# Kernel optimization log

Measured on AMD Instinct MI355X. Metric: run time of the kernel, lower is better.

The kernel has to match this reference:

```python
import jax, jax.numpy as jnp
import numpy as np

CH, K, RR = 12, 7, 4  # pooled temporal size / involution kernel / reduction ratio

def conv3d(x, w, pad):
    return jax.lax.conv_general_dilated(x, w, (1, 1, 1), [(pad, pad)] * 3,
                                        dimension_numbers=('NCDHW', 'OIDHW', 'NCDHW'))

def conv1x1(x, w, b=None):
    out = jnp.einsum('oi,bidhw->bodhw', w, x)
    return out if b is None else out + b[None, :, None, None, None]

def adaptive_pool(x, outs):
    b, c, D, H, W = x.shape
    fd, fh, fw = D // outs[0], H // outs[1], W // outs[2]
    return x.reshape(b, c, outs[0], fd, outs[1], fh, outs[2], fw).mean(axis=(3, 5, 7))

def bnorm(x, g, b):
    m = x.mean(axis=(0, 2, 3, 4), keepdims=True)
    v = x.var(axis=(0, 2, 3, 4), keepdims=True)
    return (x - m) * jax.lax.rsqrt(v + 1e-5) * g[None, :, None, None, None] + b[None, :, None, None, None]

def setup_inputs():
    key = jax.random.key(0)
    ks = jax.random.split(key, 12)
    c = 64; cr = c // RR; Cf = c + CH * cr; M = CH * K * K
    def nrm(k_, shape, fan_in):
        return jax.random.normal(k_, shape, jnp.float32) / np.sqrt(fan_in)
    return {
        'x_CT': jax.random.normal(ks[0], (2, c, 8, 56, 56), jnp.float32),
        'x_WSI': jax.random.normal(ks[1], (2, c, 12, 56, 56), jnp.float32),
        'W_ct': nrm(ks[2], (c, c), c), 'b_ct': jnp.zeros((c,), jnp.float32),
        'W_wsi': nrm(ks[3], (c, c), c), 'b_wsi': jnp.zeros((c,), jnp.float32),
        'W_att': nrm(ks[4], (1 + CH, M, 5, 5, 5), M * 125),
        'W_inv': nrm(ks[5], (K * K, M), M), 'b_inv': jnp.zeros((K * K,), jnp.float32),
        'W_rr': nrm(ks[6], (cr, c, 3, 3, 3), c * 27),
        'g1': jnp.ones((Cf,), jnp.float32), 'be1': jnp.zeros((Cf,), jnp.float32),
        'g2': jnp.ones((Cf,), jnp.float32), 'be2': jnp.zeros((Cf,), jnp.float32),
        'W_p1': nrm(ks[7], (Cf, Cf), Cf), 'b_p1': jnp.zeros((Cf,), jnp.float32),
        'W_p2': nrm(ks[8], (c, Cf), Cf), 'b_p2': jnp.zeros((c,), jnp.float32),
    }

def reference(x_CT, x_WSI, W_ct, b_ct, W_wsi, b_wsi, W_att, W_inv, b_inv, W_rr,
              g1, be1, g2, be2, W_p1, b_p1, W_p2, b_p2):
    b, c, t, h, w = x_CT.shape
    cr = c // RR
    M = CH * K * K
    x1 = conv1x1(x_CT, W_ct, b_ct)
    xw1 = adaptive_pool(conv1x1(x_WSI, W_wsi, b_wsi), (CH, K, K))       # (b,c,CH,K,K)
    # cross-modal bmm: (b, thw, c) x (b, c, M) -> (b, thw, M)
    multi = jnp.einsum('bnc,bcm->bnm', x1.reshape(b, c, t * h * w).transpose(0, 2, 1),
                       xw1.reshape(b, c, M))
    feature = multi.reshape(b, t, h, w, M).transpose(0, 4, 1, 2, 3)     # (b,M,t,h,w)
    Att = jax.nn.sigmoid(conv3d(feature, W_att, 2))                      # (b,1+CH,t,h,w)
    xw3 = conv3d(x_WSI, W_rr, 1)                                         # (b,cr,CH,h,w)
    xw5 = jnp.broadcast_to(xw3.reshape(b, cr * CH, 1, h, w), (b, cr * CH, t, h, w))
    x_FS = jnp.concatenate([x_CT, xw5], axis=1)                          # (b,Cf,t,h,w)
    Att_CT = jnp.broadcast_to(Att[:, :1], (b, c, t, h, w))
    Att_WSI = jnp.tile(Att[:, 1:].reshape(b, CH, t, h * w), (1, 1, cr, 1)).reshape(b, CH * cr, t, h, w)
    Att_FS = jnp.concatenate([Att_CT, Att_WSI], axis=1)
    x_Att = x_FS * Att_FS + x_FS
    # per-pixel dynamic kernel: (b,t,K,K,h,w)
    kern = conv1x1(feature, W_inv, b_inv).transpose(0, 2, 1, 3, 4).reshape(b, t, K, K, h, w)
    x_Att1 = jax.nn.relu(bnorm(conv1x1(x_Att, W_p1, b_p1), g1, be1))
    pad = K // 2
    xp = jnp.pad(x_Att1, ((0, 0), (0, 0), (0, 0), (pad, pad), (pad, pad)))
    out = jnp.zeros_like(x_Att1)
    for i in range(K):                                                   # fixed 7x7 involution taps
        for j in range(K):
            out = out + kern[:, None, :, i, j] * xp[:, :, :, i:i + h, j:j + w]
    return conv1x1(bnorm(out, g2, be2) + x_Att, W_p2, b_p2)
```

## Files before the change

### kernel.cpp

```cpp
#include <hip/hip_runtime.h>
#include <hip/hip_bf16.h>
#include <hip/hip_fp16.h>
#include <math.h>

typedef __hip_bfloat16 bf16;
typedef unsigned short us;
typedef __attribute__((ext_vector_type(8))) short short8v;
typedef __attribute__((ext_vector_type(4))) float f32x4;
#define DEV static __device__ __forceinline__
DEV float b2f(bf16 x){ return __bfloat162float(x); }
DEV bf16  f2b(float x){ return __float2bfloat16(x); }
DEV us    f2u(float x){ bf16 h=f2b(x); return *(us*)&h; }
DEV float u2f(us u){ return __uint_as_float(((unsigned)u)<<16); }
DEV us    f2h(float x){ __half h=__float2half(x); return *(us*)&h; }
DEV float hlo(unsigned int w){ return __half2float(__ushort_as_half((us)(w&0xffff))); }
DEV float hhi(unsigned int w){ return __half2float(__ushort_as_half((us)(w>>16))); }
DEV float ldin(const void* p, long i, int f){
  return f ? ((const float*)p)[i] : b2f(((const bf16*)p)[i]);
}

#define PP 25088

#define POOLo  3211264L
#define XW1o   3286528L
#define WXo    3361792L
#define WXTo   3569792L
#define WIXo   3825792L
#define ATTo   3832064L
#define KERNo  4484352L
#define XW3o   6942976L
#define STATo  8147200L
#define FLAGo  8149248L
#define WFo    8149264L
#define WATTFo 8267280L
#define WINVFo 9222784L
#define BF16o  9251600L
#define WRR2o  WXo
#define bX1T   3211264L
#define bXATT  8028160L
#define bY1    20873216L
#define bINV   33718272L
#define bWP1B  46563328L
#define bWP2B  46628864L
#define bW2S   46645248L
#define bXWT   bY1
#define oWCT   0
#define oBCT   4096
#define oWWSI  4160
#define oBWSI  8256
#define oWRR   8320
#define oBINV  35968
#define oWP1   36032
#define oWP2   101568
#define oBP2   117952

__global__ void k_detect(const us* raw, int* flag){
  int t = threadIdx.x;
  us u = raw[2*t];
  int e = (u>>7)&0xFF;
  int hit = (e >= 137);
  unsigned long long m = __ballot(hit);
  if(t==0) flag[0] = (__popcll(m) >= 8) ? 1 : 0;
}

__global__ void k_c2f(const void* src, float* dst, int n, const int* flag){
  int i = blockIdx.x*256+threadIdx.x; if(i>=n) return;
  dst[i] = ldin(src, i, flag[0]);
}

__global__ void k_cvt(const void* Wct,const void* bct,const void* Wwsi,const void* bwsi,
                      const void* Wrr,const void* binv,const void* Wp1,const void* Wp2,
                      const void* bp2,float* wf,const int* flag){
  int i = blockIdx.x*256 + threadIdx.x;
  int f = flag[0];
  if (i < 4096){ int co=i>>6, ci=i&63; wf[oWCT + ci*64+co] = ldin(Wct,i,f); }
  else if (i < 4160){ wf[i] = ldin(bct,i-4096,f); }
  else if (i < 8256){ wf[i] = ldin(Wwsi,i-4160,f); }
  else if (i < 8320){ wf[i] = ldin(bwsi,i-8256,f); }
  else if (i < 35968){ int l=i-8320; int co=l/1728, r=l%1728, ci=r/27, tp=r%27;
                       wf[oWRR + (ci*27+tp)*16+co] = ldin(Wrr,l,f); }
  else if (i < 36017){ wf[oBINV + (i-35968)] = ldin(binv,i-35968,f); }
  else if (i < 36032){ }
  else if (i < 101568){ int l=i-36032; int co=l>>8, ci=l&255; wf[oWP1 + ci*256+co] = ldin(Wp1,l,f); }
  else if (i < 117952){ int l=i-101568; int o=l>>8, ci=l&255; wf[oWP2 + ci*64+o] = ldin(Wp2,l,f); }
  else if (i < 118016){ int l=i-117952; if(l<64) wf[oBP2 + l] = ldin(bp2,l,f); }
}

__global__ void k_wb(const void* Wp1, const void* Wp2, us* Wp1b, us* Wp2b, const int* flag){
  int i = blockIdx.x*256+threadIdx.x;
  int f = flag[0];
  if(i<65536) Wp1b[i]=f2u(ldin(Wp1,i,f));
  else if(i<81920) Wp2b[i-65536]=f2u(ldin(Wp2,i-65536,f));
}

__global__ void k_wsit(const void* xwsi_r, const int* flag, us* xwt){
  __shared__ us tl[64*68];
  int tid=threadIdx.x; int p0=blockIdx.x*64; int d=blockIdx.y; int b=blockIdx.z;
  int f=flag[0];
  #pragma unroll
  for(int k=0;k<16;k++){
    int idx=k*256+tid; int px=idx&63, c=idx>>6;
    float v = ldin(xwsi_r, ((long)(b*64+c)*12+d)*3136 + p0+px, f);
    tl[px*68+c] = f2u(v);
  }
  __syncthreads();
  #pragma unroll
  for(int k=0;k<16;k++){
    int idx=k*256+tid; int px=idx>>6, ch=idx&63;
    xwt[((size_t)(b*12+d)*3136 + p0+px)*64 + ch] = tl[px*68+ch];
  }
}

__global__ void k_pool(const us* xwt, float* pool){
  int i = blockIdx.x*256+threadIdx.x;
  int c = i&63; int m=(i>>6)%588; int b=i/37632;
  int d=m/49, r=m%49, ii=r/7, jj=r%7;
  const us* src = xwt + ((size_t)(b*12+d)*3136 + (ii*8)*56 + jj*8)*64 + c;
  float s=0;
  for(int u=0;u<8;u++)
    for(int v=0;v<8;v++) s += u2f(src[(size_t)(u*56+v)*64]);
  pool[i] = s*(1.f/64.f);
}

__global__ void k_xw1(const float* pool, const float* wf, float* xw1){
  int i = blockIdx.x*256+threadIdx.x;
  int c = i&63; int m=(i>>6)%588; int b=i/37632;
  const float* p = pool + (b*588+m)*64;
  const float* w = wf + oWWSI + c*64;
  float s = wf[oBWSI + c];
  for(int ci=0;ci<64;ci++) s += w[ci]*p[ci];
  xw1[i]=s;
}

__global__ void k_Wx(const float* Wattf, const float* xw1, float* Wx){
  int i = blockIdx.x*256+threadIdx.x; if(i>=208000) return;
  int c=i&63; int r=i>>6; int tap=r%125; int o=(r/125)%13; int b=r/1625;
  const float* wa = Wattf + (size_t)o*588*125 + tap;
  const float* xp = xw1 + b*588*64 + c;
  float s=0;
  for(int m=0;m<588;m++) s += wa[(size_t)m*125] * xp[m*64];
  Wx[i]=s;
}

__global__ void k_Wfrag(const float* Wx, us* Wf){
  int i = blockIdx.x*256+threadIdx.x; if(i>=256000) return;
  int j=i&7; int m=(i>>3)&15; int kg=(i>>7)&3; int ch=(i>>9)&1;
  int r=i>>10; int tap=r%125; int b=r/125;
  int c = ch*32 + kg*8 + j;
  float v = (m<13) ? Wx[((size_t)(b*13+m)*125+tap)*64 + c] : 0.f;
  Wf[i] = f2u(v);
}

__global__ void k_rrfrag(const float* wf, us* Wrr2){
  int i = blockIdx.x*256+threadIdx.x; if(i>=27648) return;
  int j=i&7; int l=(i>>3)&63; int kg=(i>>9)&1; int td=i>>10;
  int m=l&15, g=l>>4;
  int c = kg*32 + g*8 + j;
  Wrr2[i] = f2u(wf[oWRR + (c*27+td)*16 + m]);
}

__global__ void k_Winvx(const float* Winvf, const float* xw1, float* Wix){
  int i = blockIdx.x*256+threadIdx.x; if(i>=6272) return;
  int kk=i%49; int c=(i/49)&63; int b=i/3136;
  const float* xp = xw1 + b*588*64 + c;
  float s=0;
  for(int m=0;m<588;m++) s += Winvf[kk*588+m] * xp[m*64];
  Wix[i]=s;
}

__global__ void k_x1(const void* xct_r, const int* flag, const float* wf, us* x1t){
  int p = blockIdx.x*256+threadIdx.x;
  int co0 = blockIdx.y*16; int b = blockIdx.z;
  float acc[16];
  #pragma unroll
  for(int o=0;o<16;o++) acc[o]=wf[oBCT+co0+o];
  int f=flag[0];
  if(f){
    const float* xp = (const float*)xct_r + (size_t)b*64*PP + p;
    for(int ci=0;ci<64;ci++){
      float xv = xp[(size_t)ci*PP];
      const float* w = wf + oWCT + ci*64 + co0;
      #pragma unroll
      for(int o=0;o<16;o++) acc[o] += w[o]*xv;
    }
  } else {
    const bf16* xp = (const bf16*)xct_r + (size_t)b*64*PP + p;
    for(int ci=0;ci<64;ci++){
      float xv = b2f(xp[(size_t)ci*PP]);
      const float* w = wf + oWCT + ci*64 + co0;
      #pragma unroll
      for(int o=0;o<16;o++) acc[o] += w[o]*xv;
    }
  }
  unsigned int pk[8];
  #pragma unroll
  for(int o2=0;o2<8;o2++)
    pk[o2] = (unsigned)f2u(acc[2*o2]) | ((unsigned)f2u(acc[2*o2+1])<<16);
  us* xo = x1t + ((size_t)(b*PP)+p)*64 + co0;
  *(uint4*)xo     = make_uint4(pk[0],pk[1],pk[2],pk[3]);
  *(uint4*)(xo+8) = make_uint4(pk[4],pk[5],pk[6],pk[7]);
}

__global__ __launch_bounds__(256) void k_att(const us* x1t, const us* Wf, float* att){
  __shared__ short xt[10368];
  int tid=threadIdx.x;
  int tile=blockIdx.x, t=blockIdx.y, b=blockIdx.z;
  int y0=(tile/7)*8, x0=(tile%7)*8;
  int w=tid>>6, l=tid&63;
  int pc=l&7, pr=(l>>3)&1, g=l>>4;
  f32x4 acc0={0,0,0,0}, acc1={0,0,0,0};
  int bbase = ((2*w+pr)*12 + pc)*72 + g*8;
  const us* Wb = Wf + (size_t)b*128000 + l*8;
  for(int dt=0;dt<5;dt++){
    int ti=t+dt-2;
    if(ti<0||ti>=8) continue;
    __syncthreads();
    for(int e=tid;e<1152;e+=256){
      int px=e>>3, q=e&7;
      int row=px/12, col=px-row*12;
      int gy=y0+row-2, gx=x0+col-2;
      uint4 v={0,0,0,0};
      if((unsigned)gy<56u && (unsigned)gx<56u)
        v = *(const uint4*)(x1t + ((size_t)(b*PP) + ti*3136 + gy*56 + gx)*64 + q*8);
      *(uint4*)&xt[px*72 + q*8] = v;
    }
    __syncthreads();
    const us* Wd = Wb + dt*25600;
    #pragma unroll
    for(int dy=0;dy<5;dy++){
      #pragma unroll
      for(int dx=0;dx<5;dx++){
        int off = bbase + dy*864 + dx*72;
        short8v a0 = *(const short8v*)(Wd + (dy*5+dx)*1024);
        short8v b0 = *(const short8v*)&xt[off];
        acc0 = __builtin_amdgcn_mfma_f32_16x16x32_bf16(a0,b0,acc0,0,0,0);
        short8v a1 = *(const short8v*)(Wd + (dy*5+dx)*1024 + 512);
        short8v b1 = *(const short8v*)&xt[off+32];
        acc1 = __builtin_amdgcn_mfma_f32_16x16x32_bf16(a1,b1,acc1,0,0,0);
      }
    }
  }
  int px=l&15; int epc=px&7, epr=px>>3;
  size_t pbase=(size_t)t*3136+(size_t)(y0+2*w+epr)*56+x0+epc;
  #pragma unroll
  for(int r=0;r<4;r++){
    int o=g*4+r;
    if(o<13){
      float s=acc0[r]+acc1[r];
      att[((size_t)b*13+o)*PP+pbase]=1.f/(1.f+__expf(-s));
    }
  }
}

__global__ void k_kern(const us* x1t, const float* Wix, const float* wf, float* kern){
  int p = blockIdx.x*256+threadIdx.x; int b=blockIdx.y;
  float acc[49];
  #pragma unroll
  for(int kk=0;kk<49;kk++) acc[kk]=wf[oBINV+kk];
  const us* xp = x1t + ((size_t)b*PP + p)*64;
  #pragma unroll
  for(int c8=0;c8<8;c8++){
    uint4 v = *(const uint4*)(xp + c8*8);
    const us* vp=(const us*)&v;
    #pragma unroll
    for(int j=0;j<8;j++){
      float xv = u2f(vp[j]);
      const float* w = Wix + (b*64+c8*8+j)*49;
      #pragma unroll
      for(int kk=0;kk<49;kk++) acc[kk]+=w[kk]*xv;
    }
  }
  float* out = kern + (size_t)b*49*PP + p;
  #pragma unroll
  for(int kk=0;kk<49;kk++) out[(size_t)kk*PP]=acc[kk];
}

__global__ __launch_bounds__(256) void k_rr(const us* xwt, const us* Wrr2, bf16* xw3){
  __shared__ short xt[7200];
  int tid=threadIdx.x;
  int tile=blockIdx.x, d=blockIdx.y, b=blockIdx.z;
  int y0=(tile/7)*8, x0=(tile%7)*8;
  int w=tid>>6, l=tid&63;
  int pc=l&7, pr=(l>>3)&1, g=l>>4;
  f32x4 acc0={0,0,0,0}, acc1={0,0,0,0};
  int bbase = ((2*w+pr)*10 + pc)*72 + g*8;
  const us* Wl = Wrr2 + l*8;
  for(int dz=0;dz<3;dz++){
    int di=d+dz-1;
    if(di<0||di>=12) continue;
    __syncthreads();
    for(int e=tid;e<800;e+=256){
      int px=e>>3, q=e&7;
      int row=px/10, col=px-row*10;
      int gy=y0+row-1, gx=x0+col-1;
      uint4 v={0,0,0,0};
      if((unsigned)gy<56u && (unsigned)gx<56u)
        v = *(const uint4*)(xwt + ((size_t)(b*12+di)*3136 + gy*56 + gx)*64 + q*8);
      *(uint4*)&xt[px*72 + q*8] = v;
    }
    __syncthreads();
    const us* Wd = Wl + dz*9216;
    #pragma unroll
    for(int tap=0;tap<9;tap++){
      int dy=tap/3, dx=tap-dy*3;
      int off = bbase + (dy*10+dx)*72;
      short8v a0 = *(const short8v*)(Wd + tap*1024);
      short8v b0 = *(const short8v*)&xt[off];
      acc0 = __builtin_amdgcn_mfma_f32_16x16x32_bf16(a0,b0,acc0,0,0,0);
      short8v a1 = *(const short8v*)(Wd + tap*1024 + 512);
      short8v b1 = *(const short8v*)&xt[off+32];
      acc1 = __builtin_amdgcn_mfma_f32_16x16x32_bf16(a1,b1,acc1,0,0,0);
    }
  }
  int px=l&15; int epc=px&7, epr=px>>3;
  size_t pp=(size_t)(y0+2*w+epr)*56 + x0+epc;
  #pragma unroll
  for(int r=0;r<4;r++){
    int o=g*4+r;
    xw3[((size_t)(b*16+o)*12+d)*3136 + pp] = f2b(acc0[r]+acc1[r]);
  }
}

__global__ void k_xatt(const void* xct_r, const int* flag, const bf16* xw3,
                       const float* att, us* xattT){
  __shared__ us tl[64*258];
  int tid=threadIdx.x; int p0=blockIdx.x*64; int b=blockIdx.y;
  int f=flag[0];
  for(int k=0;k<64;k++){
    int idx=k*256+tid; int ch=idx>>6, pp=idx&63;
    int p=p0+pp;
    float v;
    if(ch<64){
      long ix = (long)(b*64+ch)*PP+p;
      float xv;
      if(f) xv = ((const float*)xct_r)[ix]; else xv = b2f(((const bf16*)xct_r)[ix]);
      v = xv * (1.f+att[(size_t)b*13*PP+p]);
    } else {
      int q=ch-64; int co=q/12, dd=q-co*12;
      int s=p%3136;
      v = b2f(xw3[((size_t)(b*16+co)*12+dd)*3136+s]) * (1.f+att[((size_t)b*13+1+q/16)*PP+p]);
    }
    tl[pp*258+ch]=f2u(v);
  }
  __syncthreads();
  for(int k=0;k<64;k++)
    xattT[((size_t)b*PP + p0+k)*256 + tid] = tl[k*258+tid];
}

__global__ __launch_bounds__(256) void k_p1(const us* xattT, const us* Wp1b, us* y1T){
  __shared__ us wt[16384];
  int tid=threadIdx.x; int w=tid>>6, l=tid&63;
  int pt=blockIdx.x, qtr=blockIdx.y, b=blockIdx.z;
  int co0 = qtr*64;
  #pragma unroll
  for(int it=0;it<8;it++){
    int f = it*256+tid;
    int n=f>>9, kc=(f>>6)&7, lane=f&63;
    int co = co0 + n*16 + (lane&15);
    int ci = (lane>>4)*8 + kc*32;
    uint4 v = *(const uint4*)(Wp1b + (size_t)co*256 + ci);
    *(uint4*)(wt + f*8) = v;
  }
  __syncthreads();
  int p0 = pt*64 + w*16;
  const us* xa = xattT + ((size_t)b*PP + p0 + (l&15))*256 + ((l>>4)*8);
  f32x4 acc[4];
  #pragma unroll
  for(int n=0;n<4;n++) acc[n]=(f32x4){0,0,0,0};
  for(int kc=0;kc<8;kc++){
    short8v a = *(const short8v*)(xa + kc*32);
    #pragma unroll
    for(int n=0;n<4;n++){
      short8v bf = *(const short8v*)(wt + ((n*8+kc)*64 + l)*8);
      acc[n] = __builtin_amdgcn_mfma_f32_16x16x32_bf16(a,bf,acc[n],0,0,0);
    }
  }
  int col=l&15, rowb=(l>>4)*4;
  us* yo = y1T + ((size_t)b*PP + p0)*256 + co0;
  #pragma unroll
  for(int n=0;n<4;n++)
    #pragma unroll
    for(int r=0;r<4;r++)
      yo[(size_t)(rowb+r)*256 + n*16 + col] = f2u(acc[n][r]);
}

__global__ void k_stats(const us* src, float* sum, float* sq){
  int tid=threadIdx.x; int pt=blockIdx.x, b=blockIdx.y;
  const us* p = src + ((size_t)b*PP + pt*64)*256 + tid;
  float s=0,q=0;
  #pragma unroll 8
  for(int i=0;i<64;i++){ float v=u2f(p[(size_t)i*256]); s+=v; q+=v*v; }
  atomicAdd(&sum[tid],s); atomicAdd(&sq[tid],q);
}
__global__ void k_finstat(const float* sum, const float* sq, const void* g, const void* be,
                          const int* flag, float* sc, float* sh){
  int ch=threadIdx.x;
  int f=flag[0];
  float m = sum[ch]*(1.f/50176.f);
  float v = sq[ch]*(1.f/50176.f) - m*m;
  float s = ldin(g,ch,f) * rsqrtf(v+1e-5f);
  sc[ch]=s; sh[ch]=ldin(be,ch,f) - m*s;
}

__global__ __launch_bounds__(256) void k_inv(const us* y1T, const float* sc1, const float* sh1,
                                             const float* kern, us* invT){
  __shared__ __align__(16) us xt[196*72];
  int tid=threadIdx.x;
  int bx=blockIdx.x, by=blockIdx.y, bz=blockIdx.z;
  int t=bz&7, b=bz>>3;
  int y0=(bx/7)*8, x0=(bx%7)*8, c0=by*64;
  int w=tid>>6, l=tid&63;
  int ty=l>>3, tx=l&7;
  int segb = c0 + (tid&7)*8;
  float scr[8], shr[8];
  #pragma unroll
  for(int j=0;j<8;j++){ scr[j]=sc1[segb+j]; shr[j]=sh1[segb+j]; }
  for(int e=tid;e<1568;e+=256){
    int row=e>>3, seg=e&7;
    int yy=row/14, xx=row%14;
    int gy=y0+yy-3, gx=x0+xx-3;
    uint4 o4={0,0,0,0};
    if(gy>=0&&gy<56&&gx>=0&&gx<56){
      uint4 v = *(const uint4*)&y1T[((size_t)b*PP + t*3136 + gy*56+gx)*256 + c0 + seg*8];
      const us* vp=(const us*)&v;
      us r[8];
      #pragma unroll
      for(int j=0;j<8;j++){
        float x = u2f(vp[j]);
        x = x*scr[j]+shr[j]; x = x>0.f?x:0.f;
        r[j]=f2h(x);
      }
      o4 = *(const uint4*)r;
    }
    *(uint4*)&xt[row*72+seg*8]=o4;
  }
  float kr[49];
  size_t pxs=(size_t)t*3136 + (y0+ty)*56 + x0+tx;
  #pragma unroll
  for(int kk=0;kk<49;kk++) kr[kk]=kern[((size_t)b*49+kk)*PP+pxs];
  __syncthreads();
  #pragma unroll
  for(int s=0;s<2;s++){
    int sub=2*w+s;
    float acc[8];
    #pragma unroll
    for(int e=0;e<8;e++) acc[e]=0;
    for(int i=0;i<7;i++){
      #pragma unroll
      for(int j=0;j<7;j++){
        uint4 u = *(const uint4*)&xt[((ty+i)*14+tx+j)*72 + sub*8];
        float kv = kr[i*7+j];
        acc[0]+=hlo(u.x)*kv; acc[1]+=hhi(u.x)*kv;
        acc[2]+=hlo(u.y)*kv; acc[3]+=hhi(u.y)*kv;
        acc[4]+=hlo(u.z)*kv; acc[5]+=hhi(u.z)*kv;
        acc[6]+=hlo(u.w)*kv; acc[7]+=hhi(u.w)*kv;
      }
    }
    unsigned pk[4];
    #pragma unroll
    for(int e=0;e<4;e++)
      pk[e] = (unsigned)f2u(acc[2*e]) | ((unsigned)f2u(acc[2*e+1])<<16);
    *(uint4*)&invT[((size_t)b*PP+pxs)*256 + c0 + sub*8] = make_uint4(pk[0],pk[1],pk[2],pk[3]);
  }
}

__global__ void k_w2s(const float* wf, const float* sc2, const float* sh2,
                      us* W2sb, float* bias2){
  __shared__ float red[256];
  int o=blockIdx.x, ci=threadIdx.x;
  float wv = wf[oWP2 + ci*64 + o];
  W2sb[o*256+ci] = f2u(wv * sc2[ci]);
  red[ci] = wv * sh2[ci];
  __syncthreads();
  for(int st=128;st>0;st>>=1){ if(ci<st) red[ci]+=red[ci+st]; __syncthreads(); }
  if(ci==0) bias2[o] = wf[oBP2+o] + red[0];
}

__global__ __launch_bounds__(256) void k_final(const us* invT, const us* xattT,
                                               const us* W2sb, const us* Wp2b,
                                               const float* bias2, float* out){
  __shared__ us wt[32768];
  int tid=threadIdx.x; int w=tid>>6, l=tid&63;
  int pt=blockIdx.x, b=blockIdx.y;
  #pragma unroll
  for(int it=0;it<16;it++){
    int f = it*256+tid;
    int which = f>>11;
    int g = f&2047;
    int n=g>>9, kc=(g>>6)&7, lane=g&63;
    int co = n*16 + (lane&15);
    int ci = (lane>>4)*8 + kc*32;
    const us* src = which ? Wp2b : W2sb;
    uint4 v = *(const uint4*)(src + (size_t)co*256 + ci);
    *(uint4*)(wt + f*8) = v;
  }
  __syncthreads();
  int p0 = pt*64 + w*16;
  size_t abase = ((size_t)b*PP + p0 + (l&15))*256 + ((l>>4)*8);
  f32x4 acc[4];
  #pragma unroll
  for(int n=0;n<4;n++) acc[n]=(f32x4){0,0,0,0};
  for(int kc=0;kc<8;kc++){
    short8v ai = *(const short8v*)(invT + abase + kc*32);
    short8v ax = *(const short8v*)(xattT + abase + kc*32);
    #pragma unroll
    for(int n=0;n<4;n++){
      short8v b1 = *(const short8v*)(wt + ((n*8+kc)*64 + l)*8);
      acc[n] = __builtin_amdgcn_mfma_f32_16x16x32_bf16(ai,b1,acc[n],0,0,0);
      short8v b2 = *(const short8v*)(wt + 16384 + ((n*8+kc)*64 + l)*8);
      acc[n] = __builtin_amdgcn_mfma_f32_16x16x32_bf16(ax,b2,acc[n],0,0,0);
    }
  }
  int col=l&15, rowb=(l>>4)*4;
  #pragma unroll
  for(int n=0;n<4;n++){
    float bb = bias2[n*16+col];
    #pragma unroll
    for(int r=0;r<4;r++)
      out[((size_t)b*64 + n*16+col)*PP + p0 + rowb + r] = acc[n][r] + bb;
  }
}

extern "C" void kernel_launch(void* const* d_in, const int* in_sizes, int n_in,
                              void* d_out, int out_size, void* d_ws, size_t ws_size,
                              hipStream_t stream){
  const void* xct_r =d_in[0];
  const void* xwsi_r=d_in[1];
  const void* Wct =d_in[2];
  const void* bct =d_in[3];
  const void* Wwsi=d_in[4];
  const void* bwsi=d_in[5];
  const void* Watt=d_in[6];
  const void* Winv=d_in[7];
  const void* binv=d_in[8];
  const void* Wrr =d_in[9];
  const void* g1  =d_in[10];
  const void* be1 =d_in[11];
  const void* g2  =d_in[12];
  const void* be2 =d_in[13];
  const void* Wp1 =d_in[14];
  const void* Wp2 =d_in[16];
  const void* bp2 =d_in[17];
  float* ws=(float*)d_ws;
  float* pool=ws+POOLo; float* xw1=ws+XW1o;
  float* Wx=ws+WXo; float* Wix=ws+WIXo;
  float* att=ws+ATTo; float* kern=ws+KERNo;
  us* Wf=(us*)(ws+WXTo);
  us* Wrr2=(us*)(ws+WRR2o);
  bf16* xw3=(bf16*)(ws+XW3o);
  float* stat=ws+STATo; float* wf=ws+WFo;
  float* Wattf=ws+WATTFo; float* Winvf=ws+WINVFo;
  float* bias2=ws+WATTFo;
  int* flag=(int*)(ws+FLAGo);
  bf16* bfb=(bf16*)(ws+BF16o);
  us* x1t=(us*)(bfb+bX1T);
  us* xattT=(us*)(bfb+bXATT); us* y1T=(us*)(bfb+bY1); us* invT=(us*)(bfb+bINV);
  us* Wp1b=(us*)(bfb+bWP1B); us* Wp2b=(us*)(bfb+bWP2B); us* W2sb=(us*)(bfb+bW2S);
  us* xwt=(us*)(bfb+bXWT);
  float* sum1=stat; float* sq1=stat+256; float* sum2=stat+512; float* sq2=stat+768;
  float* sc1=stat+1024; float* sh1=stat+1280; float* sc2=stat+1536; float* sh2=stat+1792;

  hipMemsetAsync(stat,0,4096,stream);
  k_detect<<<1,64,0,stream>>>((const us*)xct_r,flag);
  k_c2f   <<<3733,256,0,stream>>>(Watt,Wattf,955500,flag);
  k_c2f   <<<113,256,0,stream>>>(Winv,Winvf,28812,flag);
  k_cvt   <<<461,256,0,stream>>>(Wct,bct,Wwsi,bwsi,Wrr,binv,Wp1,Wp2,bp2,wf,flag);
  k_wb    <<<320,256,0,stream>>>(Wp1,Wp2,Wp1b,Wp2b,flag);
  k_wsit  <<<dim3(49,12,2),256,0,stream>>>(xwsi_r,flag,xwt);
  k_pool  <<<294,256,0,stream>>>(xwt,pool);
  k_xw1   <<<294,256,0,stream>>>(pool,wf,xw1);
  k_Wx    <<<813,256,0,stream>>>(Wattf,xw1,Wx);
  k_Wfrag <<<1000,256,0,stream>>>(Wx,Wf);
  k_rrfrag<<<108,256,0,stream>>>(wf,Wrr2);
  k_Winvx <<<25,256,0,stream>>>(Winvf,xw1,Wix);
  k_x1    <<<dim3(98,4,2),256,0,stream>>>(xct_r,flag,wf,x1t);
  k_att   <<<dim3(49,8,2),256,0,stream>>>(x1t,Wf,att);
  k_kern  <<<dim3(98,2),256,0,stream>>>(x1t,Wix,wf,kern);
  k_rr    <<<dim3(49,12,2),256,0,stream>>>(xwt,Wrr2,xw3);
  k_xatt  <<<dim3(392,2),256,0,stream>>>(xct_r,flag,xw3,att,xattT);
  k_p1    <<<dim3(392,4,2),256,0,stream>>>(xattT,Wp1b,y1T);
  k_stats <<<dim3(392,2),256,0,stream>>>(y1T,sum1,sq1);
  k_finstat<<<1,256,0,stream>>>(sum1,sq1,g1,be1,flag,sc1,sh1);
  k_inv   <<<dim3(49,4,16),256,0,stream>>>(y1T,sc1,sh1,kern,invT);
  k_stats <<<dim3(392,2),256,0,stream>>>(invT,sum2,sq2);
  k_finstat<<<1,256,0,stream>>>(sum2,sq2,g2,be2,flag,sc2,sh2);
  k_w2s   <<<64,256,0,stream>>>(wf,sc2,sh2,W2sb,bias2);
  k_final <<<dim3(392,2),256,0,stream>>>(invT,xattT,W2sb,Wp2b,bias2,(float*)d_out);
}
```

Before: 386.2 us.

## Merge weight-prep kernels, fuse pool with xw1, split Winvx and kern for parallelism

```diff
diff --git a/kernel.cpp b/kernel.cpp
--- a/kernel.cpp
+++ b/kernel.cpp
@@ -1,6 +1,5 @@
 #include <hip/hip_runtime.h>
 #include <hip/hip_bf16.h>
-#include <hip/hip_fp16.h>
 #include <math.h>
 
 typedef __hip_bfloat16 bf16;
@@ -12,9 +11,8 @@
 DEV bf16  f2b(float x){ return __float2bfloat16(x); }
 DEV us    f2u(float x){ bf16 h=f2b(x); return *(us*)&h; }
 DEV float u2f(us u){ return __uint_as_float(((unsigned)u)<<16); }
-DEV us    f2h(float x){ __half h=__float2half(x); return *(us*)&h; }
-DEV float hlo(unsigned int w){ return __half2float(__ushort_as_half((us)(w&0xffff))); }
-DEV float hhi(unsigned int w){ return __half2float(__ushort_as_half((us)(w>>16))); }
+DEV float blo(unsigned int w){ return __uint_as_float(w<<16); }
+DEV float bhi(unsigned int w){ return __uint_as_float(w&0xffff0000u); }
 DEV float ldin(const void* p, long i, int f){
   return f ? ((const float*)p)[i] : b2f(((const bf16*)p)[i]);
 }
@@ -63,16 +61,16 @@
   if(t==0) flag[0] = (__popcll(m) >= 8) ? 1 : 0;
 }
 
-__global__ void k_c2f(const void* src, float* dst, int n, const int* flag){
-  int i = blockIdx.x*256+threadIdx.x; if(i>=n) return;
-  dst[i] = ldin(src, i, flag[0]);
-}
-
-__global__ void k_cvt(const void* Wct,const void* bct,const void* Wwsi,const void* bwsi,
-                      const void* Wrr,const void* binv,const void* Wp1,const void* Wp2,
-                      const void* bp2,float* wf,const int* flag){
+__global__ void k_prep(const void* Watt,const void* Winv,const void* Wct,const void* bct,
+                       const void* Wwsi,const void* bwsi,const void* Wrr,const void* binv,
+                       const void* Wp1,const void* Wp2,const void* bp2,
+                       float* Wattf,float* Winvf,float* wf,us* Wp1b,us* Wp2b,const int* flag){
   int i = blockIdx.x*256 + threadIdx.x;
   int f = flag[0];
+  if(i<955500) Wattf[i]=ldin(Watt,i,f);
+  if(i<28812)  Winvf[i]=ldin(Winv,i,f);
+  if(i<65536)  Wp1b[i]=f2u(ldin(Wp1,i,f));
+  else if(i<81920) Wp2b[i-65536]=f2u(ldin(Wp2,i-65536,f));
   if (i < 4096){ int co=i>>6, ci=i&63; wf[oWCT + ci*64+co] = ldin(Wct,i,f); }
   else if (i < 4160){ wf[i] = ldin(bct,i-4096,f); }
   else if (i < 8256){ wf[i] = ldin(Wwsi,i-4160,f); }
@@ -81,16 +79,12 @@
                        wf[oWRR + (ci*27+tp)*16+co] = ldin(Wrr,l,f); }
   else if (i < 36017){ wf[oBINV + (i-35968)] = ldin(binv,i-35968,f); }
   else if (i < 36032){ }
-  else if (i < 101568){ int l=i-36032; int co=l>>8, ci=l&255; wf[oWP1 + ci*256+co] = ldin(Wp1,l,f); }
-  else if (i < 117952){ int l=i-101568; int o=l>>8, ci=l&255; wf[oWP2 + ci*64+o] = ldin(Wp2,l,f); }
-  else if (i < 118016){ int l=i-117952; if(l<64) wf[oBP2 + l] = ldin(bp2,l,f); }
-}
-
-__global__ void k_wb(const void* Wp1, const void* Wp2, us* Wp1b, us* Wp2b, const int* flag){
-  int i = blockIdx.x*256+threadIdx.x;
-  int f = flag[0];
-  if(i<65536) Wp1b[i]=f2u(ldin(Wp1,i,f));
-  else if(i<81920) Wp2b[i-65536]=f2u(ldin(Wp2,i-65536,f));
+  else if (i < 118016){
+    int l=i-36032;
+    if(l<65536){ int co=l>>8, ci=l&255; wf[oWP1 + ci*256+co] = ldin(Wp1,l,f); }
+    else if(l<81920){ int l2=l-65536; int o=l2>>8, ci=l2&255; wf[oWP2 + ci*64+o] = ldin(Wp2,l2,f); }
+    else if(l<81984){ wf[oBP2 + (l-81920)] = ldin(bp2,l-81920,f); }
+  }
 }
 
 __global__ void k_wsit(const void* xwsi_r, const int* flag, us* xwt){
@@ -111,25 +105,22 @@
   }
 }
 
-__global__ void k_pool(const us* xwt, float* pool){
-  int i = blockIdx.x*256+threadIdx.x;
-  int c = i&63; int m=(i>>6)%588; int b=i/37632;
+__global__ __launch_bounds__(64) void k_poolxw1(const us* xwt, const float* wf, float* xw1){
+  __shared__ float pl[64];
+  int c=threadIdx.x; int m=blockIdx.x; int b=blockIdx.y;
   int d=m/49, r=m%49, ii=r/7, jj=r%7;
   const us* src = xwt + ((size_t)(b*12+d)*3136 + (ii*8)*56 + jj*8)*64 + c;
   float s=0;
+  #pragma unroll
   for(int u=0;u<8;u++)
+    #pragma unroll
     for(int v=0;v<8;v++) s += u2f(src[(size_t)(u*56+v)*64]);
-  pool[i] = s*(1.f/64.f);
-}
-
-__global__ void k_xw1(const float* pool, const float* wf, float* xw1){
-  int i = blockIdx.x*256+threadIdx.x;
-  int c = i&63; int m=(i>>6)%588; int b=i/37632;
-  const float* p = pool + (b*588+m)*64;
+  pl[c] = s*(1.f/64.f);
+  __syncthreads();
   const float* w = wf + oWWSI + c*64;
-  float s = wf[oBWSI + c];
-  for(int ci=0;ci<64;ci++) s += w[ci]*p[ci];
-  xw1[i]=s;
+  float o = wf[oBWSI + c];
+  for(int ci=0;ci<64;ci++) o += w[ci]*pl[ci];
+  xw1[(b*588+m)*64+c] = o;
 }
 
 __global__ void k_Wx(const float* Wattf, const float* xw1, float* Wx){
@@ -161,11 +152,13 @@
 
 __global__ void k_Winvx(const float* Winvf, const float* xw1, float* Wix){
   int i = blockIdx.x*256+threadIdx.x; if(i>=6272) return;
+  int ms = blockIdx.y;
   int kk=i%49; int c=(i/49)&63; int b=i/3136;
+  int m0=ms*74; int m1=m0+74; if(m1>588) m1=588;
   const float* xp = xw1 + b*588*64 + c;
   float s=0;
-  for(int m=0;m<588;m++) s += Winvf[kk*588+m] * xp[m*64];
-  Wix[i]=s;
+  for(int m=m0;m<m1;m++) s += Winvf[kk*588+m] * xp[m*64];
+  atomicAdd(&Wix[i], s);
 }
 
 __global__ void k_x1(const void* xct_r, const int* flag, const float* wf, us* x1t){
@@ -252,11 +245,15 @@
   }
 }
 
-__global__ void k_kern(const us* x1t, const float* Wix, const float* wf, float* kern){
-  int p = blockIdx.x*256+threadIdx.x; int b=blockIdx.y;
-  float acc[49];
-  #pragma unroll
-  for(int kk=0;kk<49;kk++) acc[kk]=wf[oBINV+kk];
+__global__ __launch_bounds__(256) void k_kern(const us* x1t, const float* Wix, const float* wf,
+                                              float* kern){
+  int tid=threadIdx.x;
+  int px=tid&63, cg=tid>>6;
+  int p = blockIdx.x*64 + px; int b=blockIdx.y;
+  int kk0 = cg*13;
+  float acc[13];
+  #pragma unroll
+  for(int t=0;t<13;t++) acc[t]=wf[oBINV+kk0+t];
   const us* xp = x1t + ((size_t)b*PP + p)*64;
   #pragma unroll
   for(int c8=0;c8<8;c8++){
@@ -265,14 +262,15 @@
     #pragma unroll
     for(int j=0;j<8;j++){
       float xv = u2f(vp[j]);
-      const float* w = Wix + (b*64+c8*8+j)*49;
+      const float* w = Wix + (b*64+c8*8+j)*49 + kk0;
       #pragma unroll
-      for(int kk=0;kk<49;kk++) acc[kk]+=w[kk]*xv;
+      for(int t=0;t<13;t++) acc[t]+=w[t]*xv;
     }
   }
   float* out = kern + (size_t)b*49*PP + p;
   #pragma unroll
-  for(int kk=0;kk<49;kk++) out[(size_t)kk*PP]=acc[kk];
+  for(int t=0;t<13;t++)
+    if(kk0+t<49) out[(size_t)(kk0+t)*PP]=acc[t];
 }
 
 __global__ __launch_bounds__(256) void k_rr(const us* xwt, const us* Wrr2, bf16* xw3){
@@ -428,7 +426,7 @@
       for(int j=0;j<8;j++){
         float x = u2f(vp[j]);
         x = x*scr[j]+shr[j]; x = x>0.f?x:0.f;
-        r[j]=f2h(x);
+        r[j]=f2u(x);
       }
       o4 = *(const uint4*)r;
     }
@@ -450,10 +448,10 @@
       for(int j=0;j<7;j++){
         uint4 u = *(const uint4*)&xt[((ty+i)*14+tx+j)*72 + sub*8];
         float kv = kr[i*7+j];
-        acc[0]+=hlo(u.x)*kv; acc[1]+=hhi(u.x)*kv;
-        acc[2]+=hlo(u.y)*kv; acc[3]+=hhi(u.y)*kv;
-        acc[4]+=hlo(u.z)*kv; acc[5]+=hhi(u.z)*kv;
-        acc[6]+=hlo(u.w)*kv; acc[7]+=hhi(u.w)*kv;
+        acc[0]+=kv*blo(u.x); acc[1]+=kv*bhi(u.x);
+        acc[2]+=kv*blo(u.y); acc[3]+=kv*bhi(u.y);
+        acc[4]+=kv*blo(u.z); acc[5]+=kv*bhi(u.z);
+        acc[6]+=kv*blo(u.w); acc[7]+=kv*bhi(u.w);
       }
     }
     unsigned pk[4];
@@ -542,7 +540,7 @@
   const void* Wp2 =d_in[16];
   const void* bp2 =d_in[17];
   float* ws=(float*)d_ws;
-  float* pool=ws+POOLo; float* xw1=ws+XW1o;
+  float* xw1=ws+XW1o;
   float* Wx=ws+WXo; float* Wix=ws+WIXo;
   float* att=ws+ATTo; float* kern=ws+KERNo;
   us* Wf=(us*)(ws+WXTo);
@@ -561,21 +559,19 @@
   float* sc1=stat+1024; float* sh1=stat+1280; float* sc2=stat+1536; float* sh2=stat+1792;
 
   hipMemsetAsync(stat,0,4096,stream);
+  hipMemsetAsync(Wix,0,6272*4,stream);
   k_detect<<<1,64,0,stream>>>((const us*)xct_r,flag);
-  k_c2f   <<<3733,256,0,stream>>>(Watt,Wattf,955500,flag);
-  k_c2f   <<<113,256,0,stream>>>(Winv,Winvf,28812,flag);
-  k_cvt   <<<461,256,0,stream>>>(Wct,bct,Wwsi,bwsi,Wrr,binv,Wp1,Wp2,bp2,wf,flag);
-  k_wb    <<<320,256,0,stream>>>(Wp1,Wp2,Wp1b,Wp2b,flag);
+  k_prep  <<<3733,256,0,stream>>>(Watt,Winv,Wct,bct,Wwsi,bwsi,Wrr,binv,Wp1,Wp2,bp2,
+                                  Wattf,Winvf,wf,Wp1b,Wp2b,flag);
   k_wsit  <<<dim3(49,12,2),256,0,stream>>>(xwsi_r,flag,xwt);
-  k_pool  <<<294,256,0,stream>>>(xwt,pool);
-  k_xw1   <<<294,256,0,stream>>>(pool,wf,xw1);
+  k_poolxw1<<<dim3(588,2),64,0,stream>>>(xwt,wf,xw1);
   k_Wx    <<<813,256,0,stream>>>(Wattf,xw1,Wx);
   k_Wfrag <<<1000,256,0,stream>>>(Wx,Wf);
   k_rrfrag<<<108,256,0,stream>>>(wf,Wrr2);
-  k_Winvx <<<25,256,0,stream>>>(Winvf,xw1,Wix);
+  k_Winvx <<<dim3(25,8),256,0,stream>>>(Winvf,xw1,Wix);
   k_x1    <<<dim3(98,4,2),256,0,stream>>>(xct_r,flag,wf,x1t);
   k_att   <<<dim3(49,8,2),256,0,stream>>>(x1t,Wf,att);
-  k_kern  <<<dim3(98,2),256,0,stream>>>(x1t,Wix,wf,kern);
+  k_kern  <<<dim3(392,2),256,0,stream>>>(x1t,Wix,wf,kern);
   k_rr    <<<dim3(49,12,2),256,0,stream>>>(xwt,Wrr2,xw3);
   k_xatt  <<<dim3(392,2),256,0,stream>>>(xct_r,flag,xw3,att,xattT);
   k_p1    <<<dim3(392,4,2),256,0,stream>>>(xattT,Wp1b,y1T);
```

Measured after the change: 890.0 us. 2.3x slower.
